# Performance work log

Hardware: AMD Instinct MI355X
Metric: run time of the kernel (lower is better)

Reference implementation:

```python
import jax, jax.numpy as jnp
import numpy as np

WH, WW = 7, 7
DIM, HEADS = 256, 8


def make_table_index(wh, ww):
    # relative coords table (log-spaced CPB input) and relative position index
    ch = np.arange(-(wh - 1), wh, dtype=np.float32)
    cw = np.arange(-(ww - 1), ww, dtype=np.float32)
    t = np.stack(np.meshgrid(ch, cw, indexing='ij'), axis=-1)[None]  # [1,2wh-1,2ww-1,2]
    t = t.copy()
    t[..., 0] /= (wh - 1)
    t[..., 1] /= (ww - 1)
    t *= 8.0
    t = np.sign(t) * np.log2(np.abs(t) + 1.0) / np.log2(8.0)
    coords = np.stack(np.meshgrid(np.arange(wh), np.arange(ww), indexing='ij'))
    cf = coords.reshape(2, -1)
    rc = (cf[:, :, None] - cf[:, None, :]).transpose(1, 2, 0).copy()  # [N,N,2]
    rc[..., 0] += wh - 1
    rc[..., 1] += ww - 1
    rc[..., 0] *= 2 * ww - 1
    idx = rc.sum(-1)
    return t.astype(np.float32), idx.astype(np.int32)


def setup_inputs() -> dict:
    key = jax.random.key(0)
    ks = jax.random.split(key, 10)
    B_, N, C, H = 2048, WH * WW, DIM, HEADS
    table, idx = make_table_index(WH, WW)
    return {
        'x': jax.random.normal(ks[0], (B_, N, C), jnp.float32),
        'mask': jnp.zeros((64, N, N), jnp.float32),
        'qkv_w': jax.random.normal(ks[1], (3 * C, C), jnp.float32) * 0.02,
        'q_bias': jnp.zeros((C,), jnp.float32),
        'v_bias': jnp.zeros((C,), jnp.float32),
        'logit_scale': jnp.full((H, 1, 1), np.log(10.0), jnp.float32),
        'cpb_w1': jax.random.normal(ks[2], (512, 2), jnp.float32) * 0.02,
        'cpb_b1': jnp.zeros((512,), jnp.float32),
        'cpb_w2': jax.random.normal(ks[3], (H, 512), jnp.float32) * 0.02,
        'proj_w': jax.random.normal(ks[4], (C, C), jnp.float32) * 0.02,
        'proj_b': jnp.zeros((C,), jnp.float32),
        'rel_coords_table': jnp.asarray(table),
        'rel_pos_index': jnp.asarray(idx),
    }


def _l2norm(t):
    return t / jnp.maximum(jnp.linalg.norm(t, axis=-1, keepdims=True), 1e-12)


def reference(x, mask, qkv_w, q_bias, v_bias, logit_scale, cpb_w1, cpb_b1,
              cpb_w2, proj_w, proj_b, rel_coords_table, rel_pos_index):
    B_, N, C = x.shape
    H = logit_scale.shape[0]
    hd = C // H
    qkv_b = jnp.concatenate([q_bias, jnp.zeros_like(v_bias), v_bias])
    qkv = (x @ qkv_w.T + qkv_b).reshape(B_, N, 3, H, hd).transpose(2, 0, 3, 1, 4)
    q, k, v = qkv[0], qkv[1], qkv[2]  # [B_,H,N,hd]
    attn = jnp.einsum('bhnd,bhmd->bhnm', _l2norm(q), _l2norm(k))
    scale = jnp.exp(jnp.minimum(logit_scale, jnp.log(jnp.float32(100.0))))  # [H,1,1]
    attn = attn * scale[None]
    # CPB MLP -> relative position bias
    table = jax.nn.relu(rel_coords_table @ cpb_w1.T + cpb_b1) @ cpb_w2.T  # [1,Th,Tw,H]
    table = table.reshape(-1, H)
    bias = table[rel_pos_index.reshape(-1)].reshape(N, N, H).transpose(2, 0, 1)
    attn = attn + 16.0 * jax.nn.sigmoid(bias)[None]
    nW = mask.shape[0]
    attn = attn.reshape(B_ // nW, nW, H, N, N) + mask[None, :, None]
    attn = jax.nn.softmax(attn.reshape(B_, H, N, N), axis=-1)
    out = jnp.einsum('bhnm,bhmd->bhnd', attn, v).transpose(0, 2, 1, 3).reshape(B_, N, C)
    return out @ proj_w.T + proj_b
```

## Files before the change

### kernel.cpp

```cpp
#include <hip/hip_runtime.h>

#define DEV __device__ __forceinline__

typedef float  f32x4  __attribute__((ext_vector_type(4)));
typedef __bf16 bf16x4 __attribute__((ext_vector_type(4)));
typedef __bf16 bf16x8 __attribute__((ext_vector_type(8)));

DEV unsigned short f2bf(float f) {
  unsigned u = __float_as_uint(f);
  u += 0x7fffu + ((u >> 16) & 1u);
  return (unsigned short)(u >> 16);
}

DEV void cp16(const void* g, void* l) {
  __builtin_amdgcn_global_load_lds((const __attribute__((address_space(1))) void*)g,
                                   (__attribute__((address_space(3))) void*)l, 16, 0, 0);
}

__global__ __launch_bounds__(64) void cpb_mlp(
    const float* __restrict__ tab, const float* __restrict__ w1,
    const float* __restrict__ b1, const float* __restrict__ w2,
    float* __restrict__ table16)
{
  int r = blockIdx.x;
  int t = threadIdx.x;
  float x0 = tab[r * 2 + 0], x1 = tab[r * 2 + 1];
  float part[8];
#pragma unroll
  for (int h = 0; h < 8; ++h) part[h] = 0.f;
  for (int j = t; j < 512; j += 64) {
    float hv = fmaxf(w1[j * 2 + 0] * x0 + w1[j * 2 + 1] * x1 + b1[j], 0.f);
#pragma unroll
    for (int h = 0; h < 8; ++h) part[h] += hv * w2[h * 512 + j];
  }
#pragma unroll
  for (int h = 0; h < 8; ++h) {
    float v = part[h];
    for (int off = 32; off > 0; off >>= 1) v += __shfl_down(v, off, 64);
    if (t == 0) table16[r * 8 + h] = 16.f / (1.f + expf(-v));
  }
}

__global__ __launch_bounds__(256) void prep_all(
    const float* __restrict__ X, unsigned short* __restrict__ Xb,
    const float* __restrict__ qkv_w, const float* __restrict__ proj_w,
    const float* __restrict__ q_bias, const float* __restrict__ v_bias,
    unsigned short* __restrict__ wq, unsigned short* __restrict__ wp,
    float* __restrict__ qkvb,
    const float* __restrict__ t16, const int* __restrict__ ridx,
    const float* __restrict__ mask, float* __restrict__ bias64,
    float* __restrict__ mask64)
{
  const int b = blockIdx.x;
  if (b < 12546) {
    size_t gid = (size_t)b * 256 + threadIdx.x;
    if (gid < 3211264) {
      const float4* xp = (const float4*)X;
      float4 f0 = xp[2 * gid], f1 = xp[2 * gid + 1];
      bf16x8 u;
      u[0] = (__bf16)f0.x; u[1] = (__bf16)f0.y; u[2] = (__bf16)f0.z; u[3] = (__bf16)f0.w;
      u[4] = (__bf16)f1.x; u[5] = (__bf16)f1.y; u[6] = (__bf16)f1.z; u[7] = (__bf16)f1.w;
      ((bf16x8*)Xb)[gid] = u;
    } else {
      bf16x8 z = {};
      ((bf16x8*)Xb)[gid] = z;
    }
  } else if (b < 13570) {
    int gid = (b - 12546) * 256 + threadIdx.x;
    if (gid < 196608) wq[gid] = f2bf(qkv_w[gid]);
    else              wp[gid - 196608] = f2bf(proj_w[gid - 196608]);
    if (gid < 768)
      qkvb[gid] = (gid < 256) ? q_bias[gid] : ((gid < 512) ? 0.f : v_bias[gid - 512]);
  } else {
    const float L2E = 1.44269504f;
    int gid = (b - 13570) * 256 + threadIdx.x;
    int p = gid & 4095, i = p >> 6, j = p & 63;
    bool valid = (i < 49) && (j < 49);
    if (gid < 32768) {
      int h = gid >> 12;
      bias64[gid] = valid ? t16[ridx[i * 49 + j] * 8 + h] * L2E : -1e30f;
    } else {
      int g2 = gid - 32768;
      int w = g2 >> 12;
      mask64[g2] = valid ? mask[w * 2401 + i * 49 + j] * L2E : 0.f;
    }
  }
}

__global__ __launch_bounds__(512, 2) void qkv_attn(
    const unsigned short* __restrict__ Xb, const unsigned short* __restrict__ W,
    const float* __restrict__ qkvb, const float* __restrict__ logit_scale,
    const float* __restrict__ bias64, const float* __restrict__ mask64,
    unsigned short* __restrict__ aout)
{
  __shared__ __align__(1024) char smem[65536];
  const int t = threadIdx.x, w = t >> 6, l = t & 63, quad = l >> 4, l15 = l & 15;
  char* sX = smem;
  char* vT = smem + 32768 + w * 4096;
  const int win = blockIdx.x;
  const unsigned short* xrow = Xb + (size_t)(win * 49) * 256;
  const int h = w;

  {
    const int r0 = w * 8;
    const int s = l & 31;
#pragma unroll
    for (int seg = 0; seg < 4; ++seg) {
      const int row = r0 + 2 * seg + (l >> 5);
      if (row < 49) {
        const unsigned short* src = xrow + (size_t)row * 256
                                  + (s >> 3) * 64 + (((s & 7) ^ (row & 7)) * 8);
        cp16(src, sX + (r0 + 2 * seg) * 512);
      } else {
        uint4 z = {};
        *(uint4*)(sX + row * 512 + s * 16) = z;
      }
    }
  }
  __syncthreads();

  auto do_gemm = [&](int wrb, f32x4 (&acc)[2][4]) {
    bf16x8 wreg[2][8];
#pragma unroll
    for (int nt = 0; nt < 2; ++nt) {
      const unsigned short* wr = W + (size_t)(wrb + nt * 16 + l15) * 256;
#pragma unroll
      for (int c = 0; c < 8; ++c)
        wreg[nt][c] = *(const bf16x8*)(wr + (c >> 1) * 64 + (4 * (c & 1) + quad) * 8);
    }
#pragma unroll
    for (int kt = 0; kt < 4; ++kt)
#pragma unroll
      for (int kk = 0; kk < 2; ++kk) {
        bf16x8 xf[4];
#pragma unroll
        for (int mA = 0; mA < 4; ++mA)
          xf[mA] = *(const bf16x8*)(sX + (mA * 16 + l15) * 512 + kt * 128
                                       + (((4 * kk + quad) ^ (l15 & 7)) * 16));
#pragma unroll
        for (int nt = 0; nt < 2; ++nt)
#pragma unroll
          for (int mA = 0; mA < 4; ++mA)
            acc[nt][mA] = __builtin_amdgcn_mfma_f32_16x16x32_bf16(
                wreg[nt][kt * 2 + kk], xf[mA], acc[nt][mA], 0, 0, 0);
      }
  };

  auto cvt_norm = [&](f32x4 (&acc)[2][4], const float* bias, float mul,
                      bf16x8 (&f)[4]) {
    const f32x4 b0 = *(const f32x4*)(bias + quad * 4);
    const f32x4 b1 = *(const f32x4*)(bias + 16 + quad * 4);
#pragma unroll
    for (int mt = 0; mt < 4; ++mt) {
      float v[8];
#pragma unroll
      for (int r = 0; r < 4; ++r) {
        v[r]     = acc[0][mt][r] + b0[r];
        v[4 + r] = acc[1][mt][r] + b1[r];
      }
      float ss = 0.f;
#pragma unroll
      for (int i = 0; i < 8; ++i) ss += v[i] * v[i];
      ss += __shfl_xor(ss, 16, 64); ss += __shfl_xor(ss, 32, 64);
      const float rn = mul / fmaxf(sqrtf(ss), 1e-12f);
#pragma unroll
      for (int i = 0; i < 8; ++i) f[mt][i] = (__bf16)(v[i] * rn);
    }
  };

  const float scale = __expf(fminf(logit_scale[h], 4.60517019f)) * 1.44269504f;
  bf16x8 kf[4], qf[4];
  {
    f32x4 ka[2][4] = {};
    do_gemm(256 + h * 32, ka);
    cvt_norm(ka, qkvb + 256 + h * 32, 1.f, kf);
  }
  {
    f32x4 qa[2][4] = {};
    do_gemm(h * 32, qa);
    cvt_norm(qa, qkvb + h * 32, scale, qf);
  }

  f32x4 sacc[4][4] = {};
  __builtin_amdgcn_s_setprio(1);
#pragma unroll
  for (int mt = 0; mt < 4; ++mt)
#pragma unroll
    for (int nt = 0; nt < 4; ++nt)
      sacc[mt][nt] = __builtin_amdgcn_mfma_f32_16x16x32_bf16(kf[mt], qf[nt], sacc[mt][nt], 0, 0, 0);
  __builtin_amdgcn_s_setprio(0);

  {
    f32x4 va[2][4] = {};
    do_gemm(512 + h * 32, va);
    const f32x4 vb0 = *(const f32x4*)(qkvb + 512 + h * 32 + quad * 4);
    const f32x4 vb1 = *(const f32x4*)(qkvb + 512 + h * 32 + 16 + quad * 4);
#pragma unroll
    for (int mA = 0; mA < 4; ++mA) {
      const int tok = mA * 16 + l15;
#pragma unroll
      for (int nt = 0; nt < 2; ++nt) {
#pragma unroll
        for (int r = 0; r < 4; ++r) {
          const int d = nt * 16 + quad * 4 + r;
          *(__bf16*)(vT + d * 128 + (((tok >> 3) ^ (d & 7)) << 4) + (tok & 7) * 2) =
              (__bf16)(va[nt][mA][r] + (nt ? vb1[r] : vb0[r]));
        }
      }
    }
  }

  const float* bh = bias64 + (size_t)h * 4096;
  const float* mw = mask64 + (size_t)(win & 63) * 4096;
  uint2 pk2[4][4];
  float rs4[4];
#pragma unroll
  for (int nt = 0; nt < 4; ++nt) {
    const int i = nt * 16 + l15;
    float mx = -3e38f;
#pragma unroll
    for (int mt = 0; mt < 4; ++mt) {
      const int jb = mt * 16 + quad * 4;
      const f32x4 b4 = *(const f32x4*)(bh + i * 64 + jb);
      const f32x4 m4 = *(const f32x4*)(mw + i * 64 + jb);
#pragma unroll
      for (int r = 0; r < 4; ++r) {
        float sv = sacc[mt][nt][r] + b4[r] + m4[r];
        sacc[mt][nt][r] = sv;
        mx = fmaxf(mx, sv);
      }
    }
    mx = fmaxf(mx, __shfl_xor(mx, 16, 64));
    mx = fmaxf(mx, __shfl_xor(mx, 32, 64));
    float sum = 0.f;
#pragma unroll
    for (int mt = 0; mt < 4; ++mt) {
      float pv[4];
#pragma unroll
      for (int r = 0; r < 4; ++r) {
        pv[r] = __builtin_amdgcn_exp2f(sacc[mt][nt][r] - mx);
        sum += pv[r];
      }
      bf16x4 pk;
      pk[0] = (__bf16)pv[0]; pk[1] = (__bf16)pv[1];
      pk[2] = (__bf16)pv[2]; pk[3] = (__bf16)pv[3];
      pk2[nt][mt] = *(uint2*)&pk;
    }
    sum += __shfl_xor(sum, 16, 64);
    sum += __shfl_xor(sum, 32, 64);
    rs4[nt] = 1.f / sum;
  }

  asm volatile("s_waitcnt lgkmcnt(0)" ::: "memory");
  __builtin_amdgcn_sched_barrier(0);
  bf16x8 vf[2][2];
#pragma unroll
  for (int kk = 0; kk < 2; ++kk)
#pragma unroll
    for (int mt = 0; mt < 2; ++mt)
      vf[kk][mt] = *(const bf16x8*)(vT + (mt * 16 + l15) * 128
                                       + (((4 * kk + quad) ^ (l15 & 7)) * 16));

  const int srcA = l15 + 32 * (quad & 1);
  const bool hiSel = (quad >> 1) != 0;
  f32x4 oacc[2][4] = {};
#pragma unroll
  for (int kk = 0; kk < 2; ++kk) {
    bf16x8 pf[4];
#pragma unroll
    for (int nt = 0; nt < 4; ++nt) {
      const uint2 e = pk2[nt][2 * kk], o = pk2[nt][2 * kk + 1];
      unsigned e0 = __shfl((int)e.x, srcA, 64),      e1 = __shfl((int)e.y, srcA, 64);
      unsigned o0 = __shfl((int)o.x, srcA, 64),      o1 = __shfl((int)o.y, srcA, 64);
      unsigned e2 = __shfl((int)e.x, srcA + 16, 64), e3 = __shfl((int)e.y, srcA + 16, 64);
      unsigned o2 = __shfl((int)o.x, srcA + 16, 64), o3 = __shfl((int)o.y, srcA + 16, 64);
      uint4 u;
      u.x = hiSel ? o0 : e0; u.y = hiSel ? o1 : e1;
      u.z = hiSel ? o2 : e2; u.w = hiSel ? o3 : e3;
      pf[nt] = *(bf16x8*)&u;
    }
    __builtin_amdgcn_s_setprio(1);
#pragma unroll
    for (int mt = 0; mt < 2; ++mt)
#pragma unroll
      for (int nt = 0; nt < 4; ++nt)
        oacc[mt][nt] = __builtin_amdgcn_mfma_f32_16x16x32_bf16(vf[kk][mt], pf[nt], oacc[mt][nt], 0, 0, 0);
    __builtin_amdgcn_s_setprio(0);
  }

  unsigned short* ob = aout + (size_t)(win * 8 + h) * 1568;
#pragma unroll
  for (int nt = 0; nt < 4; ++nt) {
    const int tok = nt * 16 + l15;
    if (tok < 49) {
      unsigned short* op = ob + tok * 32;
      const float rs = rs4[nt];
#pragma unroll
      for (int mt = 0; mt < 2; ++mt) {
        bf16x4 ov;
        ov[0] = (__bf16)(oacc[mt][nt][0] * rs); ov[1] = (__bf16)(oacc[mt][nt][1] * rs);
        ov[2] = (__bf16)(oacc[mt][nt][2] * rs); ov[3] = (__bf16)(oacc[mt][nt][3] * rs);
        *(bf16x4*)(op + mt * 16 + quad * 4) = ov;
      }
    }
  }
}

__global__ __launch_bounds__(256) void gemm_proj(
    const unsigned short* __restrict__ A, const unsigned short* __restrict__ W,
    const float* __restrict__ bias, float* __restrict__ Y)
{
  __shared__ __align__(1024) unsigned short sA[128 * 64];
  __shared__ __align__(1024) unsigned short sB[128 * 64];
  const int t = threadIdx.x, w = t >> 6, l = t & 63, quad = l >> 4, l15 = l & 15;
  const int bm = blockIdx.y * 128, bn = blockIdx.x * 128;
  const int wm = (w >> 1) * 64, wn = (w & 1) * 64;
  const int srow = t >> 3, sch = t & 7;
  const int sc = sch ^ (srow & 7);

  size_t abase[4];
#pragma unroll
  for (int i = 0; i < 4; ++i) {
    const int g = bm + i * 32 + srow;
    const unsigned wn_ = (unsigned)(((unsigned long long)g * 87652394ull) >> 32);
    const int tok = g - (int)wn_ * 49;
    abase[i] = ((size_t)wn_ * 8 + (sc >> 2)) * 1568 + (size_t)tok * 32 + (sc & 3) * 8;
  }

  f32x4 acc[4][4] = {};
  for (int kt = 0; kt < 4; ++kt) {
    const int k0 = kt << 6;
    if (kt) __syncthreads();
#pragma unroll
    for (int i = 0; i < 4; ++i) {
      const int row = i * 32 + srow;
      cp16(A + abase[i] + (size_t)kt * 2 * 1568, sA + (i * 256 + w * 64) * 8);
      cp16(W + (size_t)(bn + row) * 256 + k0 + sc * 8, sB + (i * 256 + w * 64) * 8);
    }
    __syncthreads();
#pragma unroll
    for (int kk = 0; kk < 2; ++kk) {
      bf16x8 xf[4], wf[4];
#pragma unroll
      for (int mt = 0; mt < 4; ++mt)
        xf[mt] = *(const bf16x8*)&sA[(wm + mt * 16 + l15) * 64 + (((4 * kk + quad) ^ (l15 & 7)) * 8)];
#pragma unroll
      for (int nt = 0; nt < 4; ++nt)
        wf[nt] = *(const bf16x8*)&sB[(wn + nt * 16 + l15) * 64 + (((4 * kk + quad) ^ (l15 & 7)) * 8)];
#pragma unroll
      for (int nt = 0; nt < 4; ++nt)
#pragma unroll
        for (int mt = 0; mt < 4; ++mt)
          acc[nt][mt] = __builtin_amdgcn_mfma_f32_16x16x32_bf16(wf[nt], xf[mt], acc[nt][mt], 0, 0, 0);
    }
  }
#pragma unroll
  for (int mA = 0; mA < 4; ++mA) {
    const int row = bm + wm + mA * 16 + l15;
    float* orow = Y + (size_t)row * 256;
#pragma unroll
    for (int nW = 0; nW < 4; ++nW) {
      const int c0 = bn + wn + nW * 16 + quad * 4;
      const f32x4 bv = *(const f32x4*)(bias + c0);
      f32x4 v = acc[nW][mA];
      v[0] += bv[0]; v[1] += bv[1]; v[2] += bv[2]; v[3] += bv[3];
      *(f32x4*)(orow + c0) = v;
    }
  }
}

extern "C" void kernel_launch(void* const* d_in, const int* in_sizes, int n_in,
                              void* d_out, int out_size, void* d_ws, size_t ws_size,
                              hipStream_t stream) {
  const float* x           = (const float*)d_in[0];
  const float* mask        = (const float*)d_in[1];
  const float* qkv_w       = (const float*)d_in[2];
  const float* q_bias      = (const float*)d_in[3];
  const float* v_bias      = (const float*)d_in[4];
  const float* logit_scale = (const float*)d_in[5];
  const float* cpb_w1      = (const float*)d_in[6];
  const float* cpb_b1      = (const float*)d_in[7];
  const float* cpb_w2      = (const float*)d_in[8];
  const float* proj_w      = (const float*)d_in[9];
  const float* proj_b      = (const float*)d_in[10];
  const float* rel_tab     = (const float*)d_in[11];
  const int*   rel_idx     = (const int*)d_in[12];
  float*       out         = (float*)d_out;

  char* ws = (char*)d_ws;
  unsigned short* xbf     = (unsigned short*)(ws + 0);
  unsigned short* aows    = (unsigned short*)(ws + 154140672);
  unsigned short* wq      = (unsigned short*)(ws + 205520896);
  unsigned short* wp      = (unsigned short*)(ws + 205914112);
  float*          qkvb    = (float*)(ws + 206045184);
  float*          table16 = (float*)(ws + 206048256);
  float*          bias64  = (float*)(ws + 206053888);
  float*          mask64  = (float*)(ws + 206184960);

  cpb_mlp<<<169, 64, 0, stream>>>(rel_tab, cpb_w1, cpb_b1, cpb_w2, table16);
  prep_all<<<14722, 256, 0, stream>>>(x, xbf, qkv_w, proj_w, q_bias, v_bias,
                                      wq, wp, qkvb, table16, rel_idx, mask,
                                      bias64, mask64);
  qkv_attn<<<2048, 512, 0, stream>>>(xbf, wq, qkvb, logit_scale, bias64, mask64, aows);
  gemm_proj<<<dim3(2, 784), 256, 0, stream>>>(aows, wp, proj_b, out);
}
```

Before: 410.7 us.

## Fuse output projection GEMM into attention kernel via shared-memory staging

Removes the separate gemm_proj kernel. Each attention block now writes its normalized per-head outputs into shared memory (reusing the X buffer with an XOR-swizzled layout), synchronizes, and runs the projection GEMM with the existing do_gemm helper, each warp producing 32 output columns. The bf16 attention-output round trip through global memory and one kernel launch go away. In exchange the block adds an extra barrier and reloads projection weights per block instead of sharing them across a 128x128 tile.

```diff
diff --git a/kernel.cpp b/kernel.cpp
--- a/kernel.cpp
+++ b/kernel.cpp
@@ -89,9 +89,10 @@
 
 __global__ __launch_bounds__(512, 2) void qkv_attn(
     const unsigned short* __restrict__ Xb, const unsigned short* __restrict__ W,
-    const float* __restrict__ qkvb, const float* __restrict__ logit_scale,
+    const unsigned short* __restrict__ Wp, const float* __restrict__ qkvb,
+    const float* __restrict__ proj_b, const float* __restrict__ logit_scale,
     const float* __restrict__ bias64, const float* __restrict__ mask64,
-    unsigned short* __restrict__ aout)
+    float* __restrict__ out)
 {
   __shared__ __align__(1024) char smem[65536];
   const int t = threadIdx.x, w = t >> 6, l = t & 63, quad = l >> 4, l15 = l & 15;
@@ -119,11 +120,11 @@
   }
   __syncthreads();
 
-  auto do_gemm = [&](int wrb, f32x4 (&acc)[2][4]) {
+  auto do_gemm = [&](const unsigned short* Wsrc, int wrb, f32x4 (&acc)[2][4]) {
     bf16x8 wreg[2][8];
 #pragma unroll
     for (int nt = 0; nt < 2; ++nt) {
-      const unsigned short* wr = W + (size_t)(wrb + nt * 16 + l15) * 256;
+      const unsigned short* wr = Wsrc + (size_t)(wrb + nt * 16 + l15) * 256;
 #pragma unroll
       for (int c = 0; c < 8; ++c)
         wreg[nt][c] = *(const bf16x8*)(wr + (c >> 1) * 64 + (4 * (c & 1) + quad) * 8);
@@ -172,12 +173,12 @@
   bf16x8 kf[4], qf[4];
   {
     f32x4 ka[2][4] = {};
-    do_gemm(256 + h * 32, ka);
+    do_gemm(W, 256 + h * 32, ka);
     cvt_norm(ka, qkvb + 256 + h * 32, 1.f, kf);
   }
   {
     f32x4 qa[2][4] = {};
-    do_gemm(h * 32, qa);
+    do_gemm(W, h * 32, qa);
     cvt_norm(qa, qkvb + h * 32, scale, qf);
   }
 
@@ -192,7 +193,7 @@
 
   {
     f32x4 va[2][4] = {};
-    do_gemm(512 + h * 32, va);
+    do_gemm(W, 512 + h * 32, va);
     const f32x4 vb0 = *(const f32x4*)(qkvb + 512 + h * 32 + quad * 4);
     const f32x4 vb1 = *(const f32x4*)(qkvb + 512 + h * 32 + 16 + quad * 4);
 #pragma unroll
@@ -209,6 +210,7 @@
       }
     }
   }
+  __syncthreads();
 
   const float* bh = bias64 + (size_t)h * 4096;
   const float* mw = mask64 + (size_t)(win & 63) * 4096;
@@ -251,8 +253,6 @@
     rs4[nt] = 1.f / sum;
   }
 
-  asm volatile("s_waitcnt lgkmcnt(0)" ::: "memory");
-  __builtin_amdgcn_sched_barrier(0);
   bf16x8 vf[2][2];
 #pragma unroll
   for (int kk = 0; kk < 2; ++kk)
@@ -288,83 +288,44 @@
     __builtin_amdgcn_s_setprio(0);
   }
 
-  unsigned short* ob = aout + (size_t)(win * 8 + h) * 1568;
-#pragma unroll
-  for (int nt = 0; nt < 4; ++nt) {
-    const int tok = nt * 16 + l15;
-    if (tok < 49) {
-      unsigned short* op = ob + tok * 32;
+  {
+    char* sOx = smem;
+    const int ktp = h >> 1;
+#pragma unroll
+    for (int nt = 0; nt < 4; ++nt) {
+      const int tok = nt * 16 + l15;
       const float rs = rs4[nt];
 #pragma unroll
       for (int mt = 0; mt < 2; ++mt) {
+        const int col = h * 32 + mt * 16 + quad * 4;
+        const int cc = (col >> 3) & 7;
         bf16x4 ov;
         ov[0] = (__bf16)(oacc[mt][nt][0] * rs); ov[1] = (__bf16)(oacc[mt][nt][1] * rs);
         ov[2] = (__bf16)(oacc[mt][nt][2] * rs); ov[3] = (__bf16)(oacc[mt][nt][3] * rs);
-        *(bf16x4*)(op + mt * 16 + quad * 4) = ov;
-      }
-    }
-  }
-}
-
-__global__ __launch_bounds__(256) void gemm_proj(
-    const unsigned short* __restrict__ A, const unsigned short* __restrict__ W,
-    const float* __restrict__ bias, float* __restrict__ Y)
-{
-  __shared__ __align__(1024) unsigned short sA[128 * 64];
-  __shared__ __align__(1024) unsigned short sB[128 * 64];
-  const int t = threadIdx.x, w = t >> 6, l = t & 63, quad = l >> 4, l15 = l & 15;
-  const int bm = blockIdx.y * 128, bn = blockIdx.x * 128;
-  const int wm = (w >> 1) * 64, wn = (w & 1) * 64;
-  const int srow = t >> 3, sch = t & 7;
-  const int sc = sch ^ (srow & 7);
-
-  size_t abase[4];
-#pragma unroll
-  for (int i = 0; i < 4; ++i) {
-    const int g = bm + i * 32 + srow;
-    const unsigned wn_ = (unsigned)(((unsigned long long)g * 87652394ull) >> 32);
-    const int tok = g - (int)wn_ * 49;
-    abase[i] = ((size_t)wn_ * 8 + (sc >> 2)) * 1568 + (size_t)tok * 32 + (sc & 3) * 8;
-  }
-
-  f32x4 acc[4][4] = {};
-  for (int kt = 0; kt < 4; ++kt) {
-    const int k0 = kt << 6;
-    if (kt) __syncthreads();
-#pragma unroll
-    for (int i = 0; i < 4; ++i) {
-      const int row = i * 32 + srow;
-      cp16(A + abase[i] + (size_t)kt * 2 * 1568, sA + (i * 256 + w * 64) * 8);
-      cp16(W + (size_t)(bn + row) * 256 + k0 + sc * 8, sB + (i * 256 + w * 64) * 8);
-    }
-    __syncthreads();
-#pragma unroll
-    for (int kk = 0; kk < 2; ++kk) {
-      bf16x8 xf[4], wf[4];
-#pragma unroll
-      for (int mt = 0; mt < 4; ++mt)
-        xf[mt] = *(const bf16x8*)&sA[(wm + mt * 16 + l15) * 64 + (((4 * kk + quad) ^ (l15 & 7)) * 8)];
-#pragma unroll
-      for (int nt = 0; nt < 4; ++nt)
-        wf[nt] = *(const bf16x8*)&sB[(wn + nt * 16 + l15) * 64 + (((4 * kk + quad) ^ (l15 & 7)) * 8)];
-#pragma unroll
-      for (int nt = 0; nt < 4; ++nt)
-#pragma unroll
-        for (int mt = 0; mt < 4; ++mt)
-          acc[nt][mt] = __builtin_amdgcn_mfma_f32_16x16x32_bf16(wf[nt], xf[mt], acc[nt][mt], 0, 0, 0);
-    }
-  }
+        *(bf16x4*)(sOx + tok * 512 + ktp * 128 + ((cc ^ (tok & 7)) << 4)
+                   + (quad & 1) * 8) = ov;
+      }
+    }
+  }
+  __syncthreads();
+
+  f32x4 pacc[2][4] = {};
+  do_gemm(Wp, h * 32, pacc);
+
+  const f32x4 pb0 = *(const f32x4*)(proj_b + h * 32 + quad * 4);
+  const f32x4 pb1 = *(const f32x4*)(proj_b + h * 32 + 16 + quad * 4);
 #pragma unroll
   for (int mA = 0; mA < 4; ++mA) {
-    const int row = bm + wm + mA * 16 + l15;
-    float* orow = Y + (size_t)row * 256;
-#pragma unroll
-    for (int nW = 0; nW < 4; ++nW) {
-      const int c0 = bn + wn + nW * 16 + quad * 4;
-      const f32x4 bv = *(const f32x4*)(bias + c0);
-      f32x4 v = acc[nW][mA];
-      v[0] += bv[0]; v[1] += bv[1]; v[2] += bv[2]; v[3] += bv[3];
-      *(f32x4*)(orow + c0) = v;
+    const int tok = mA * 16 + l15;
+    if (tok < 49) {
+      float* orow = out + (size_t)(win * 49 + tok) * 256 + h * 32;
+#pragma unroll
+      for (int nt = 0; nt < 2; ++nt) {
+        f32x4 v = pacc[nt][mA];
+        const f32x4 pb = nt ? pb1 : pb0;
+        v[0] += pb[0]; v[1] += pb[1]; v[2] += pb[2]; v[3] += pb[3];
+        *(f32x4*)(orow + nt * 16 + quad * 4) = v;
+      }
     }
   }
 }
@@ -389,7 +350,6 @@
 
   char* ws = (char*)d_ws;
   unsigned short* xbf     = (unsigned short*)(ws + 0);
-  unsigned short* aows    = (unsigned short*)(ws + 154140672);
   unsigned short* wq      = (unsigned short*)(ws + 205520896);
   unsigned short* wp      = (unsigned short*)(ws + 205914112);
   float*          qkvb    = (float*)(ws + 206045184);
@@ -401,6 +361,6 @@
   prep_all<<<14722, 256, 0, stream>>>(x, xbf, qkv_w, proj_w, q_bias, v_bias,
                                       wq, wp, qkvb, table16, rel_idx, mask,
                                       bias64, mask64);
-  qkv_attn<<<2048, 512, 0, stream>>>(xbf, wq, qkvb, logit_scale, bias64, mask64, aows);
-  gemm_proj<<<dim3(2, 784), 256, 0, stream>>>(aows, wp, proj_b, out);
-}
+  qkv_attn<<<2048, 512, 0, stream>>>(xbf, wq, wp, qkvb, proj_b, logit_scale,
+                                     bias64, mask64, out);
+}
```

Result: slower. 419.2 us (+2.1%).
